# Kernel optimization log

Measured on AMD Instinct MI355X. Metric: run time of the kernel, lower is better.

Reference implementation:

```python
import jax, jax.numpy as jnp
import numpy as np

NUM_CLASSES = 1
STRIDES = (8, 16, 32)
CENTER_RADIUS = 2.5
REG_W, OBJ_W, CLS_W, LMK_W = 5.0, 1.0, 1.0, 5.0
BETA = 1.0 / 9.0   # SmoothL1 beta
BIG = 1e9          # mask-out cost for non-fg anchors / invalid GTs


def _bce_logits(x, t):
    # BCEWithLogits: softplus(x) - x*t (stable)
    return jax.nn.softplus(x) - x * t


def _smooth_l1(d):
    a = jnp.abs(d)
    return jnp.where(a < BETA, 0.5 * a * a / BETA, a - 0.5 * BETA)


def _make_grids(hw_list):
    gs, ss = [], []
    for (h, w), s in zip(hw_list, STRIDES):
        yv, xv = jnp.meshgrid(jnp.arange(h), jnp.arange(w), indexing='ij')
        g = jnp.stack([xv, yv], -1).reshape(-1, 2).astype(jnp.float32)
        gs.append(g)
        ss.append(jnp.full((g.shape[0],), float(s), jnp.float32))
    return jnp.concatenate(gs, 0), jnp.concatenate(ss, 0)


def _flat(p):
    b, c = p.shape[0], p.shape[1]
    return p.transpose(0, 2, 3, 1).reshape(b, -1, c)


def _pairwise_iou(a, b):
    # a [G,4] xyxy, b [A,4] xyxy -> [G,A]
    tl = jnp.maximum(a[:, None, :2], b[None, :, :2])
    br = jnp.minimum(a[:, None, 2:], b[None, :, 2:])
    wh = jnp.clip(br - tl, 0.0)
    inter = wh[..., 0] * wh[..., 1]
    aa = (a[:, 2] - a[:, 0]) * (a[:, 3] - a[:, 1])
    ab = (b[:, 2] - b[:, 0]) * (b[:, 3] - b[:, 1])
    return inter / (aa[:, None] + ab[None, :] - inter + 1e-8)


def _giou(a, b):
    # elementwise GIoU, a,b [N,4] xyxy -> [N]
    tl = jnp.maximum(a[:, :2], b[:, :2]); br = jnp.minimum(a[:, 2:], b[:, 2:])
    wh = jnp.clip(br - tl, 0.0); inter = wh[:, 0] * wh[:, 1]
    aa = (a[:, 2] - a[:, 0]) * (a[:, 3] - a[:, 1])
    ab = (b[:, 2] - b[:, 0]) * (b[:, 3] - b[:, 1])
    union = aa + ab - inter
    iou = inter / (union + 1e-8)
    ctl = jnp.minimum(a[:, :2], b[:, :2]); cbr = jnp.maximum(a[:, 2:], b[:, 2:])
    cwh = jnp.clip(cbr - ctl, 0.0); carea = cwh[:, 0] * cwh[:, 1]
    return iou - (carea - union) / (carea + 1e-8)


def _assign(boxes, cls, obj, gt_boxes, gt_labels, gt_valid, grids, strides):
    # SimOTA, masked/jittable form. boxes [A,4], cls [A,C], obj [A,1], gt_* [G,...]
    G = gt_boxes.shape[0]
    xys = (grids + 0.5) * strides[:, None]  # [A,2] anchor centers
    dl = xys[None, :, 0] - gt_boxes[:, None, 0]
    dr = gt_boxes[:, None, 2] - xys[None, :, 0]
    dt = xys[None, :, 1] - gt_boxes[:, None, 1]
    db = gt_boxes[:, None, 3] - xys[None, :, 1]
    in_box = (jnp.minimum(jnp.minimum(dl, dr), jnp.minimum(dt, db)) > 0.0) & gt_valid[:, None]
    cx = (gt_boxes[:, 0] + gt_boxes[:, 2]) * 0.5
    cy = (gt_boxes[:, 1] + gt_boxes[:, 3]) * 0.5
    rad = CENTER_RADIUS * strides[None, :]
    cdl = xys[None, :, 0] - (cx[:, None] - rad)
    cdr = cx[:, None] + rad - xys[None, :, 0]
    cdt = xys[None, :, 1] - (cy[:, None] - rad)
    cdb = cy[:, None] + rad - xys[None, :, 1]
    in_ctr = (jnp.minimum(jnp.minimum(cdl, cdr), jnp.minimum(cdt, cdb)) > 0.0) & gt_valid[:, None]
    fg = jnp.any(in_box, 0) | jnp.any(in_ctr, 0)  # [A] candidate anchors
    in_both = in_box & in_ctr
    ious = _pairwise_iou(gt_boxes, boxes) * fg[None, :].astype(boxes.dtype)  # [G,A]
    topk = jax.lax.top_k(ious, 10)[0]
    dyn_k = jnp.maximum(topk.sum(1).astype(jnp.int32), 1)  # dynamic-k per GT
    p = jnp.sqrt(jax.nn.sigmoid(cls) * jax.nn.sigmoid(obj))  # [A,C]
    t = jax.nn.one_hot(gt_labels, NUM_CLASSES)               # [G,C]
    logp = jnp.clip(jnp.log(p), -100.0)
    log1mp = jnp.clip(jnp.log(1.0 - p), -100.0)
    cls_cost = -(t[:, None, :] * logp[None] + (1.0 - t[:, None, :]) * log1mp[None]).sum(-1)
    cost = (cls_cost - 3.0 * jnp.log(ious + 1e-8)
            + 1e5 * (~in_both) + BIG * (~fg)[None, :] + BIG * (~gt_valid)[:, None])
    # rank-based smallest-k selection == topk(largest=False)
    ranks = jnp.argsort(jnp.argsort(cost, 1), 1)
    matching = (ranks < dyn_k[:, None]) & fg[None, :] & gt_valid[:, None]
    # conflict resolution: anchor matched to >1 GT keeps argmin-cost GT
    multi = matching.sum(0) > 1
    keep = jnp.arange(G)[:, None] == jnp.argmin(cost, 0)[None, :]
    matching = jnp.where(multi[None, :], keep, matching)
    fg_final = jnp.any(matching, 0)
    matched_gt = jnp.argmax(matching, 0)
    pred_ious = (matching.astype(boxes.dtype) * ious).sum(0)
    return fg_final, matched_gt, pred_ious


def _image_loss(boxes, cls, obj, lmk, gt_boxes, gt_labels, gt_lmk, gt_valid, grids, strides):
    fg, mgt, pious = _assign(boxes, cls, obj, gt_boxes, gt_labels, gt_valid, grids, strides)
    fgf = fg.astype(boxes.dtype)
    loss_obj = _bce_logits(obj[:, 0], fgf).sum()
    cls_t = jax.nn.one_hot(gt_labels[mgt], NUM_CLASSES) * pious[:, None]
    loss_cls = (_bce_logits(cls, cls_t) * fgf[:, None]).sum()
    loss_iou = ((1.0 - _giou(boxes, gt_boxes[mgt])) * fgf).sum()
    lmk_t = gt_lmk[mgt]  # [A,5,2]
    vm = ((lmk_t[..., 0] >= 0) & (lmk_t[..., 1] >= 0) & fg[:, None]).astype(boxes.dtype)
    loss_lmk = (_smooth_l1(lmk - lmk_t) * vm[..., None]).sum() / jnp.maximum(vm.sum(), 1.0)
    return loss_iou, loss_obj, loss_cls, loss_lmk, fgf.sum()


def _forward(cls0, reg0, obj0, lmk0, cls1, reg1, obj1, lmk1, cls2, reg2, obj2, lmk2,
             gt_boxes, gt_landmarks, gt_labels, gt_valid):
    hw = [(c.shape[2], c.shape[3]) for c in (cls0, cls1, cls2)]
    grids, strides = _make_grids(hw)
    cls_p = jnp.concatenate([_flat(cls0), _flat(cls1), _flat(cls2)], 1)  # [B,A,C]
    reg_p = jnp.concatenate([_flat(reg0), _flat(reg1), _flat(reg2)], 1)  # [B,A,4]
    obj_p = jnp.concatenate([_flat(obj0), _flat(obj1), _flat(obj2)], 1)  # [B,A,1]
    lmk_p = jnp.concatenate([_flat(lmk0), _flat(lmk1), _flat(lmk2)], 1)  # [B,A,10]
    b, A = reg_p.shape[0], reg_p.shape[1]
    xy = (reg_p[..., :2] + grids[None]) * strides[None, :, None]
    wh = jnp.exp(reg_p[..., 2:]) * strides[None, :, None]
    boxes = jnp.concatenate([xy - 0.5 * wh, xy + 0.5 * wh], -1)  # xyxy [B,A,4]
    lmk = (lmk_p.reshape(b, A, 5, 2) + grids[None, :, None, :]) * strides[None, :, None, None]
    li, lo, lc, ll, nfg = jax.vmap(_image_loss, in_axes=(0, 0, 0, 0, 0, 0, 0, 0, None, None))(
        boxes, cls_p, obj_p, lmk, gt_boxes, gt_labels, gt_landmarks, gt_valid, grids, strides)
    num_fg = jnp.maximum(nfg.sum(), 1.0)
    liou = REG_W * li.sum() / num_fg
    lobj = OBJ_W * lo.sum() / num_fg
    lcls = CLS_W * lc.sum() / num_fg
    llmk = LMK_W * ll.sum() / num_fg
    return liou + lobj + lcls + llmk, liou, lobj, lcls, llmk


def setup_inputs() -> dict:
    key = jax.random.key(0)
    ks = jax.random.split(key, 18)
    B, G = 16, 50
    d = {}
    for i, (h, w) in enumerate([(80, 80), (40, 40), (20, 20)]):
        d[f'cls{i}'] = jax.random.normal(ks[4 * i + 0], (B, NUM_CLASSES, h, w), jnp.float32)
        d[f'reg{i}'] = jax.random.normal(ks[4 * i + 1], (B, 4, h, w), jnp.float32)
        d[f'obj{i}'] = jax.random.normal(ks[4 * i + 2], (B, 1, h, w), jnp.float32)
        d[f'lmk{i}'] = jax.random.normal(ks[4 * i + 3], (B, 10, h, w), jnp.float32)
    cx = jax.random.uniform(ks[12], (B, G), minval=48.0, maxval=592.0)
    cy = jax.random.uniform(ks[13], (B, G), minval=48.0, maxval=592.0)
    wd = jax.random.uniform(ks[14], (B, G, 2), minval=12.0, maxval=96.0)
    d['gt_boxes'] = jnp.stack([cx - wd[..., 0] / 2, cy - wd[..., 1] / 2,
                               cx + wd[..., 0] / 2, cy + wd[..., 1] / 2], -1)
    u = jax.random.uniform(ks[15], (B, G, 5, 2))
    pts = d['gt_boxes'][..., None, :2] + u * wd[..., None, :]
    inv = jax.random.uniform(ks[16], (B, G, 5)) < 0.15  # some invisible landmarks
    d['gt_landmarks'] = jnp.where(inv[..., None], -1.0, pts)
    d['gt_labels'] = jnp.zeros((B, G), jnp.int32)  # single class (face)
    d['gt_valid'] = jnp.ones((B, G), bool)
    return d


def reference(cls0, reg0, obj0, lmk0, cls1, reg1, obj1, lmk1, cls2, reg2, obj2, lmk2,
              gt_boxes, gt_landmarks, gt_labels, gt_valid):
    return _forward(cls0, reg0, obj0, lmk0, cls1, reg1, obj1, lmk1, cls2, reg2, obj2, lmk2,
                    gt_boxes, gt_landmarks, gt_labels, gt_valid)
```

## Files before the change

### kernel.cpp

```cpp
#include <hip/hip_runtime.h>
#include <math.h>

#define NB 16
#define NA 8400
#define NG 50
#define TK 10
#define SELT 256
#define LP 11
#define NCHUNK 33
#define FGB 2
#define MCAP 512

#define CTR_FG(b)  ((b)*64)
#define CTR_M(b)   ((b)*64 + 16)
#define CTR_FD     (16*64)

__device__ __forceinline__ float sigmoidf_(float x){ return 1.f/(1.f+expf(-x)); }
__device__ __forceinline__ float softplusf_(float x){ return log1pf(expf(-fabsf(x))) + fmaxf(x, 0.f); }
__device__ __forceinline__ float bce_(float x, float t){ return softplusf_(x) - x*t; }
__device__ __forceinline__ float sl1_(float d){
    const float B = 1.f/9.f;
    float a = fabsf(d);
    return a < B ? 0.5f*a*a/B : a - 0.5f*B;
}

__device__ __forceinline__ void anchor_geom(int a, int& lvl, int& hw, int& gx, int& gy, float& st){
    if (a < 6400){ lvl=0; hw=a;      gx=hw%80; gy=hw/80; st=8.f; }
    else if (a < 8000){ lvl=1; hw=a-6400; gx=hw%40; gy=hw/40; st=16.f; }
    else { lvl=2; hw=a-8000; gx=hw%20; gy=hw/20; st=32.f; }
}

__device__ __forceinline__ float giou_(float4 a, float4 b){
    float tlx = fmaxf(a.x,b.x), tly = fmaxf(a.y,b.y);
    float brx = fminf(a.z,b.z), bry = fminf(a.w,b.w);
    float iw = fmaxf(brx-tlx,0.f), ih = fmaxf(bry-tly,0.f);
    float inter = iw*ih;
    float aa = (a.z-a.x)*(a.w-a.y);
    float ab = (b.z-b.x)*(b.w-b.y);
    float uni = aa + ab - inter;
    float iou = inter / (uni + 1e-8f);
    float ctlx = fminf(a.x,b.x), ctly = fminf(a.y,b.y);
    float cbrx = fmaxf(a.z,b.z), cbry = fmaxf(a.w,b.w);
    float cw = fmaxf(cbrx-ctlx,0.f), ch = fmaxf(cbry-ctly,0.f);
    float ca = cw*ch;
    return iou - (ca - uni) / (ca + 1e-8f);
}

__global__ void __launch_bounds__(256) k_decode(
    const float* __restrict__ cls0, const float* __restrict__ reg0, const float* __restrict__ obj0, const float* __restrict__ lmk0,
    const float* __restrict__ cls1, const float* __restrict__ reg1, const float* __restrict__ obj1, const float* __restrict__ lmk1,
    const float* __restrict__ cls2, const float* __restrict__ reg2, const float* __restrict__ obj2, const float* __restrict__ lmk2,
    const float* __restrict__ gtb, const unsigned char* __restrict__ gtv_raw, unsigned char* __restrict__ gtv,
    int* __restrict__ fgList, int* __restrict__ posOf, int* __restrict__ ctr,
    float4* __restrict__ boxC, float4* __restrict__ metaC,
    float* __restrict__ ccPC, float* __restrict__ ccNC,
    float* __restrict__ lmkC, float2* __restrict__ ocC,
    int4* __restrict__ mstate, double* __restrict__ pObj)
{
    __shared__ float4 sgb[NG];
    __shared__ unsigned char sval[NG];
    __shared__ int sIsByte;
    __shared__ int swc[4];
    __shared__ int sbase;
    __shared__ double sred[256];
    int b = blockIdx.y;
    int tid = threadIdx.x;
    int a = blockIdx.x * 256 + tid;
    bool act = (a < NA);

    int lvl, hw, gx, gy; float st = 0.f;
    float rx=0.f, ry=0.f, rw=0.f, rh=0.f, cl=0.f, ob=0.f, lmv[10];
    #pragma unroll
    for (int k = 0; k < 10; k++) lmv[k] = 0.f;
    if (act){
        anchor_geom(a, lvl, hw, gx, gy, st);
        const float* cp = lvl==0?cls0:(lvl==1?cls1:cls2);
        const float* rp = lvl==0?reg0:(lvl==1?reg1:reg2);
        const float* op = lvl==0?obj0:(lvl==1?obj1:obj2);
        const float* lp = lvl==0?lmk0:(lvl==1?lmk1:lmk2);
        int HW = lvl==0?6400:(lvl==1?1600:400);
        rx = rp[(b*4+0)*HW+hw]; ry = rp[(b*4+1)*HW+hw];
        rw = rp[(b*4+2)*HW+hw]; rh = rp[(b*4+3)*HW+hw];
        cl = cp[b*HW+hw]; ob = op[b*HW+hw];
        #pragma unroll
        for (int k = 0; k < 10; k++) lmv[k] = lp[(b*10+k)*HW+hw];
    }

    if (tid == 0) sIsByte = 0;
    if (tid < NG){
        const float* gp = &gtb[(size_t)(b*NG+tid)*4];
        sgb[tid] = make_float4(gp[0], gp[1], gp[2], gp[3]);
    }
    __syncthreads();
    {
        int any = 0;
        for (int i = tid; i < NB*NG; i += 256) if ((i & 3) && gtv_raw[i]) any = 1;
        if (any) sIsByte = 1;
    }
    __syncthreads();
    if (tid < NG){
        unsigned char vv = sIsByte ? (gtv_raw[b*NG+tid] != 0) : (gtv_raw[4*(b*NG+tid)] != 0);
        sval[tid] = vv;
        if (blockIdx.x == 0) gtv[b*NG+tid] = vv;
    }
    __syncthreads();

    double so = 0.0;
    bool f = false;
    float4 bx; float ax=0.f, ay=0.f, r=0.f, abv=0.f, ccPv=0.f, ccNv=0.f;
    float lmc[10];
    if (act){
        int idx = b*NA + a;
        float xc = (rx + (float)gx) * st, yc = (ry + (float)gy) * st;
        float wd = expf(rw) * st, ht = expf(rh) * st;
        bx = make_float4(xc - 0.5f*wd, yc - 0.5f*ht, xc + 0.5f*wd, yc + 0.5f*ht);
        abv = (bx.z - bx.x) * (bx.w - bx.y);
        so = (double)softplusf_(ob);
        float p = sqrtf(sigmoidf_(cl) * sigmoidf_(ob));
        ccPv = -fmaxf(logf(p), -100.f);
        ccNv = -fmaxf(logf(1.f - p), -100.f);
        #pragma unroll
        for (int k = 0; k < 5; k++){
            lmc[2*k]   = (lmv[2*k]   + (float)gx) * st;
            lmc[2*k+1] = (lmv[2*k+1] + (float)gy) * st;
        }
        mstate[idx] = make_int4(0, 0x7fffffff, 0, 0);
        ax = ((float)gx + 0.5f) * st; ay = ((float)gy + 0.5f) * st;
        r = 2.5f * st;
        for (int g = 0; g < NG; g++){
            if (!__ballot(!f)) break;
            if (!sval[g]) continue;
            float4 gv = sgb[g];
            bool inb = fminf(fminf(ax-gv.x, gv.z-ax), fminf(ay-gv.y, gv.w-ay)) > 0.f;
            float cx = (gv.x+gv.z)*0.5f, cy = (gv.y+gv.w)*0.5f;
            bool inc = fminf(fminf(ax-(cx-r), (cx+r)-ax), fminf(ay-(cy-r), (cy+r)-ay)) > 0.f;
            f = f || inb || inc;
        }
    }

    unsigned long long m = __ballot(f);
    int wave = tid >> 6, lane = tid & 63;
    if (lane == 0) swc[wave] = __popcll(m);
    __syncthreads();
    if (tid == 0){
        int tot = swc[0] + swc[1] + swc[2] + swc[3];
        sbase = tot ? atomicAdd(&ctr[CTR_FG(b)], tot) : 0;
    }
    __syncthreads();
    if (f){
        int wbase = sbase;
        for (int w = 0; w < 4; w++) if (w < wave) wbase += swc[w];
        int pos = wbase + __popcll(m & ((1ull << lane) - 1ull));
        fgList[b*NA + pos] = a;
        posOf[b*NA + a] = pos;
        boxC[b*NA + pos] = bx;
        metaC[b*NA + pos] = make_float4(ax, ay, r, abv);
        ccPC[b*NA + pos] = ccPv;
        ccNC[b*NA + pos] = ccNv;
        ocC[b*NA + pos] = make_float2(ob, cl);
        #pragma unroll
        for (int k = 0; k < 10; k++) lmkC[(size_t)(b*NA + pos)*10 + k] = lmc[k];
    }

    sred[tid] = so;
    for (int off = 128; off >= 1; off >>= 1){
        __syncthreads();
        if (tid < off) sred[tid] += sred[tid+off];
    }
    if (tid == 0) pObj[b*NCHUNK + blockIdx.x] = sred[0];
}

__global__ void __launch_bounds__(SELT) k_select(
    const int* __restrict__ fgList, const int* __restrict__ posOf, int* __restrict__ ctr,
    const float4* __restrict__ boxC, const float4* __restrict__ metaC,
    const float* __restrict__ ccPC, const float* __restrict__ ccNC,
    const float* __restrict__ gtb, const int* __restrict__ gtl, const unsigned char* __restrict__ gtv,
    int4* __restrict__ mstate, int* __restrict__ mList)
{
    int bg = blockIdx.x;
    int b = bg / NG, g = bg - b*NG;
    if (!gtv[b*NG+g]) return;
    int tid = threadIdx.x;

    __shared__ float sIou[SELT*LP];
    __shared__ unsigned long long sK[SELT*LP];
    __shared__ int sDk;

    const float* gp = &gtb[(size_t)(b*NG+g)*4];
    float4 gb = make_float4(gp[0], gp[1], gp[2], gp[3]);
    bool lab0 = (gtl[b*NG+g] == 0);
    int nf = ctr[CTR_FG(b)];

    float ag = (gb.z - gb.x) * (gb.w - gb.y);
    float cx = (gb.x + gb.z) * 0.5f, cy = (gb.y + gb.w) * 0.5f;

    const float4* bC = boxC  + (size_t)b*NA;
    const float4* mC = metaC + (size_t)b*NA;
    const float*  cS = (lab0 ? ccPC : ccNC) + (size_t)b*NA;
    const int*    fL = fgList + (size_t)b*NA;

    float mi[TK]; unsigned long long mk[TK];
    #pragma unroll
    for (int k = 0; k < TK; k++){ mi[k] = 0.f; mk[k] = 0xFFFFFFFFFFFFFFFFull; }

    int i = tid;
    float4 bxv, mt; float ccv; unsigned int ia;
    if (i < nf){ bxv = bC[i]; mt = mC[i]; ccv = cS[i]; ia = (unsigned int)fL[i]; }
    while (i < nf){
        int i2 = i + SELT;
        float4 bxv2, mt2; float ccv2; unsigned int ia2;
        if (i2 < nf){ bxv2 = bC[i2]; mt2 = mC[i2]; ccv2 = cS[i2]; ia2 = (unsigned int)fL[i2]; }
        float tlx = fmaxf(gb.x, bxv.x), tly = fmaxf(gb.y, bxv.y);
        float brx = fminf(gb.z, bxv.z), bry = fminf(gb.w, bxv.w);
        float iw = fmaxf(brx - tlx, 0.f), ih = fmaxf(bry - tly, 0.f);
        float inter = iw * ih;
        float im = inter / (ag + mt.w - inter + 1e-8f);
        float ax = mt.x, ay = mt.y, r = mt.z;
        bool inb = fminf(fminf(ax-gb.x, gb.z-ax), fminf(ay-gb.y, gb.w-ay)) > 0.f;
        bool inc = fminf(fminf(ax-(cx-r), (cx+r)-ax), fminf(ay-(cy-r), (cy+r)-ay)) > 0.f;
        float c = ccv - 3.f * logf(im + 1e-8f);
        if (!(inb && inc)) c += 1e5f;
        if (im > mi[TK-1]){
            float v = im;
            #pragma unroll
            for (int k = 0; k < TK; k++){
                if (v > mi[k]){ float t = mi[k]; mi[k] = v; v = t; }
            }
        }
        unsigned int fb = __float_as_uint(c);
        unsigned int ck = fb ^ ((unsigned int)((int)fb >> 31) | 0x80000000u);
        unsigned long long key = ((unsigned long long)ck << 32) | ia;
        if (key < mk[TK-1]){
            unsigned long long kv = key;
            #pragma unroll
            for (int k = 0; k < TK; k++){
                if (kv < mk[k]){ unsigned long long t = mk[k]; mk[k] = kv; kv = t; }
            }
        }
        i = i2; bxv = bxv2; mt = mt2; ccv = ccv2; ia = ia2;
    }

    #pragma unroll
    for (int k = 0; k < TK; k++){
        sIou[tid*LP+k] = mi[k];
        sK[tid*LP+k] = mk[k];
    }

    for (int off = SELT/2; off >= 1; off >>= 1){
        __syncthreads();
        if (tid < off){
            {
                float* Al = &sIou[tid*LP]; float* Bl = &sIou[(tid+off)*LP];
                float r2[TK]; int ii = 0, jj = 0;
                for (int k = 0; k < TK; k++){
                    bool ta = (jj >= TK) || (ii < TK && Al[ii] >= Bl[jj]);
                    r2[k] = ta ? Al[ii++] : Bl[jj++];
                }
                for (int k = 0; k < TK; k++) Al[k] = r2[k];
            }
            {
                unsigned long long* Ak = &sK[tid*LP]; unsigned long long* Bk = &sK[(tid+off)*LP];
                unsigned long long rk[TK]; int ii = 0, jj = 0;
                for (int k = 0; k < TK; k++){
                    bool ta = (jj >= TK) || (ii < TK && Ak[ii] <= Bk[jj]);
                    rk[k] = ta ? Ak[ii++] : Bk[jj++];
                }
                for (int k = 0; k < TK; k++) Ak[k] = rk[k];
            }
        }
    }
    __syncthreads();
    if (tid == 0){
        float s = 0.f;
        for (int k = 0; k < TK; k++) s += sIou[k];
        int dk = (int)s;
        if (dk < 1) dk = 1;
        if (dk > TK) dk = TK;
        sDk = dk;
    }
    __syncthreads();
    int dk = sDk;
    if (tid < dk){
        unsigned long long kk = sK[tid];
        unsigned int a = (unsigned int)(kk & 0xFFFFFFFFull);
        if (a < (unsigned int)NA){
            int pos = posOf[b*NA + (int)a];
            int* mp = (int*)&mstate[b*NA + (int)a];
            int old = atomicAdd(mp, 1);
            if (old == 0){
                int p = atomicAdd(&ctr[CTR_M(b)], 1);
                mList[b*MCAP + p] = (int)a;
            }
            atomicMin(mp + 1, g);
            float4 bxv = boxC[b*NA + pos];
            float4 mt = metaC[b*NA + pos];
            float tlx = fmaxf(gb.x, bxv.x), tly = fmaxf(gb.y, bxv.y);
            float brx = fminf(gb.z, bxv.z), bry = fminf(gb.w, bxv.w);
            float iw = fmaxf(brx - tlx, 0.f), ih = fmaxf(bry - tly, 0.f);
            float inter = iw * ih;
            float im = inter / (ag + mt.w - inter + 1e-8f);
            atomicAdd((float*)(mp + 2), im);
        }
    }
}

__global__ void __launch_bounds__(256) k_fg_loss(
    const float4* __restrict__ boxC, const float4* __restrict__ metaC,
    const float* __restrict__ ccPC, const float* __restrict__ ccNC,
    const float* __restrict__ lmkC, const float2* __restrict__ ocC,
    const int* __restrict__ posOf, const int4* __restrict__ mstate,
    const int* __restrict__ mList, int* __restrict__ ctr,
    const float* __restrict__ gtb, const float* __restrict__ gtlm, const int* __restrict__ gtl,
    const unsigned char* __restrict__ gtv, double* __restrict__ partials,
    const double* __restrict__ pObj, float* __restrict__ out)
{
    __shared__ float4 sgb[NG];
    __shared__ int slab[NG];
    __shared__ unsigned char sval[NG];
    __shared__ float slmk[NG*10];
    int b = blockIdx.y;
    int tid = threadIdx.x;
    if (tid < NG){
        const float* gp = &gtb[(size_t)(b*NG+tid)*4];
        sgb[tid] = make_float4(gp[0], gp[1], gp[2], gp[3]);
        slab[tid] = gtl[b*NG+tid];
        sval[tid] = gtv[b*NG+tid];
    }
    for (int i = tid; i < NG*10; i += 256) slmk[i] = gtlm[(size_t)b*NG*10 + i];
    __syncthreads();

    int n = ctr[CTR_M(b)];
    double lo = 0, lc = 0, li = 0, lnum = 0, lden = 0, nfg = 0;

    for (int i = blockIdx.x*256 + tid; i < n; i += FGB*256){
        int a = mList[b*MCAP + i];
        int pos = posOf[b*NA + a];
        int4 ms = mstate[b*NA + a];
        float4 bx = boxC[b*NA + pos];
        float4 mt = metaC[b*NA + pos];
        float2 oc = ocC[b*NA + pos];
        float pious; int m;
        if (ms.x == 1){ m = ms.y; pious = __int_as_float(ms.z); }
        else {
            float ax = mt.x, ay = mt.y, r = mt.z, ab = mt.w;
            float cp = ccPC[b*NA + pos], cn = ccNC[b*NA + pos];
            float bestC = INFINITY, bestIou = 0.f; int bestG = 0;
            for (int g = 0; g < NG; g++){
                float4 gbv = sgb[g];
                int valid = sval[g];
                float tlx = fmaxf(gbv.x, bx.x), tly = fmaxf(gbv.y, bx.y);
                float brx = fminf(gbv.z, bx.z), bry = fminf(gbv.w, bx.w);
                float iw = fmaxf(brx - tlx, 0.f), ih = fmaxf(bry - tly, 0.f);
                float inter = iw * ih;
                float agv = (gbv.z - gbv.x) * (gbv.w - gbv.y);
                float im = inter / (agv + ab - inter + 1e-8f);
                bool inb = (fminf(fminf(ax-gbv.x, gbv.z-ax), fminf(ay-gbv.y, gbv.w-ay)) > 0.f) && valid;
                float cxg = (gbv.x + gbv.z) * 0.5f, cyg = (gbv.y + gbv.w) * 0.5f;
                bool inc = (fminf(fminf(ax-(cxg-r), (cxg+r)-ax), fminf(ay-(cyg-r), (cyg+r)-ay)) > 0.f) && valid;
                float cc = (slab[g] == 0) ? cp : cn;
                float c = cc - 3.f * logf(im + 1e-8f);
                if (!(inb && inc)) c += 1e5f;
                if (!valid) c += 1e9f;
                if (c < bestC){ bestC = c; bestG = g; bestIou = im; }
            }
            m = bestG; pious = bestIou;
        }
        lo += (double)(-oc.x);
        float tgt = (slab[m] == 0) ? pious : 0.f;
        lc += (double)bce_(oc.y, tgt);
        li += (double)(1.f - giou_(bx, sgb[m]));
        #pragma unroll
        for (int k = 0; k < 5; k++){
            float tx = slmk[m*10 + 2*k];
            float ty = slmk[m*10 + 2*k + 1];
            if (tx >= 0.f && ty >= 0.f){
                lnum += (double)(sl1_(lmkC[(size_t)(b*NA+pos)*10 + 2*k] - tx)
                               + sl1_(lmkC[(size_t)(b*NA+pos)*10 + 2*k + 1] - ty));
                lden += 1.0;
            }
        }
        nfg += 1.0;
    }

    __shared__ double s[6*256];
    s[0*256+tid] = lo; s[1*256+tid] = lc; s[2*256+tid] = li;
    s[3*256+tid] = lnum; s[4*256+tid] = lden; s[5*256+tid] = nfg;
    for (int off = 128; off >= 1; off >>= 1){
        __syncthreads();
        if (tid < off){
            #pragma unroll
            for (int q = 0; q < 6; q++) s[q*256+tid] += s[q*256+tid+off];
        }
    }
    if (tid == 0){
        #pragma unroll
        for (int q = 0; q < 6; q++) partials[(b*FGB + blockIdx.x)*6 + q] = s[q*256];
    }

    __threadfence();
    __shared__ int sLast;
    if (tid == 0) sLast = (atomicAdd(&ctr[CTR_FD], 1) == NB*FGB - 1);
    __syncthreads();
    if (!sLast) return;

    __shared__ double sf[NB][5];
    if (tid < NB){
        double flo = 0, flc = 0, fli = 0, fln = 0, fld = 0, fnf = 0;
        for (int ch = 0; ch < NCHUNK; ch++) flo += pObj[tid*NCHUNK + ch];
        for (int blk = 0; blk < FGB; blk++){
            const double* p = &partials[(tid*FGB + blk)*6];
            flo += p[0]; flc += p[1]; fli += p[2];
            fln += p[3]; fld += p[4]; fnf += p[5];
        }
        sf[tid][0] = flo; sf[tid][1] = flc; sf[tid][2] = fli;
        sf[tid][3] = fln / fmax(fld, 1.0); sf[tid][4] = fnf;
    }
    __syncthreads();
    if (tid == 0){
        double flo = 0, flc = 0, fli = 0, fll = 0, fnfg = 0;
        for (int bb = 0; bb < NB; bb++){
            flo += sf[bb][0]; flc += sf[bb][1]; fli += sf[bb][2]; fll += sf[bb][3]; fnfg += sf[bb][4];
        }
        double nf2 = fmax(fnfg, 1.0);
        double liou = 5.0 * fli / nf2;
        double lobj = 1.0 * flo / nf2;
        double lcls = 1.0 * flc / nf2;
        double llmk = 5.0 * fll / nf2;
        out[0] = (float)(liou + lobj + lcls + llmk);
        out[1] = (float)liou;
        out[2] = (float)lobj;
        out[3] = (float)lcls;
        out[4] = (float)llmk;
    }
}

extern "C" void kernel_launch(void* const* d_in, const int* in_sizes, int n_in,
                              void* d_out, int out_size, void* d_ws, size_t ws_size,
                              hipStream_t stream) {
    const float* cls0 = (const float*)d_in[0];
    const float* reg0 = (const float*)d_in[1];
    const float* obj0 = (const float*)d_in[2];
    const float* lmk0 = (const float*)d_in[3];
    const float* cls1 = (const float*)d_in[4];
    const float* reg1 = (const float*)d_in[5];
    const float* obj1 = (const float*)d_in[6];
    const float* lmk1 = (const float*)d_in[7];
    const float* cls2 = (const float*)d_in[8];
    const float* reg2 = (const float*)d_in[9];
    const float* obj2 = (const float*)d_in[10];
    const float* lmk2 = (const float*)d_in[11];
    const float* gtb  = (const float*)d_in[12];
    const float* gtlm = (const float*)d_in[13];
    const int*   gtl  = (const int*)d_in[14];
    const unsigned char* gtv_raw = (const unsigned char*)d_in[15];
    float* out = (float*)d_out;

    char* ws = (char*)d_ws;
    size_t off = 0;
    float4* boxC  = (float4*)(ws + off); off += (size_t)NB*NA*sizeof(float4);
    float4* metaC = (float4*)(ws + off); off += (size_t)NB*NA*sizeof(float4);
    int4* mstate  = (int4*)(ws + off);   off += (size_t)NB*NA*sizeof(int4);
    float* lmkC = (float*)(ws + off); off += (size_t)NB*NA*10*sizeof(float);
    float2* ocC = (float2*)(ws + off); off += (size_t)NB*NA*sizeof(float2);
    float* ccPC = (float*)(ws + off); off += (size_t)NB*NA*sizeof(float);
    float* ccNC = (float*)(ws + off); off += (size_t)NB*NA*sizeof(float);
    int* fgList = (int*)(ws + off);   off += (size_t)NB*NA*sizeof(int);
    int* posOf  = (int*)(ws + off);   off += (size_t)NB*NA*sizeof(int);
    int* mList  = (int*)(ws + off);   off += (size_t)NB*MCAP*sizeof(int);
    int* ctr    = (int*)(ws + off);   off += (size_t)8192;
    double* pObj = (double*)(ws + off); off += (size_t)NB*NCHUNK*sizeof(double);
    double* partials = (double*)(ws + off); off += (size_t)NB*FGB*6*sizeof(double);
    unsigned char* gtv = (unsigned char*)(ws + off); off += (size_t)NB*NG;

    hipMemsetAsync(ctr, 0, 8192, stream);

    dim3 grdA(NCHUNK, NB);
    k_decode<<<grdA, dim3(256), 0, stream>>>(cls0, reg0, obj0, lmk0, cls1, reg1, obj1, lmk1,
                                             cls2, reg2, obj2, lmk2, gtb, gtv_raw, gtv,
                                             fgList, posOf, ctr, boxC, metaC, ccPC, ccNC,
                                             lmkC, ocC, mstate, pObj);

    k_select<<<dim3(NB*NG), dim3(SELT), 0, stream>>>(fgList, posOf, ctr, boxC, metaC, ccPC, ccNC,
                                                     gtb, gtl, gtv, mstate, mList);

    k_fg_loss<<<dim3(FGB, NB), dim3(256), 0, stream>>>(boxC, metaC, ccPC, ccNC, lmkC, ocC,
                                                       posOf, mstate, mList, ctr,
                                                       gtb, gtlm, gtl, gtv, partials,
                                                       pObj, out);
}
```

Before: 76.75 us.

## Compact mstate by fg position, transpose landmark buffer, deepen select prefetch

Result: slower. 79.21 us (+3.2%).

```diff
diff --git a/kernel.cpp b/kernel.cpp
--- a/kernel.cpp
+++ b/kernel.cpp
@@ -110,7 +110,6 @@
     float4 bx; float ax=0.f, ay=0.f, r=0.f, abv=0.f, ccPv=0.f, ccNv=0.f;
     float lmc[10];
     if (act){
-        int idx = b*NA + a;
         float xc = (rx + (float)gx) * st, yc = (ry + (float)gy) * st;
         float wd = expf(rw) * st, ht = expf(rh) * st;
         bx = make_float4(xc - 0.5f*wd, yc - 0.5f*ht, xc + 0.5f*wd, yc + 0.5f*ht);
@@ -124,7 +123,6 @@
             lmc[2*k]   = (lmv[2*k]   + (float)gx) * st;
             lmc[2*k+1] = (lmv[2*k+1] + (float)gy) * st;
         }
-        mstate[idx] = make_int4(0, 0x7fffffff, 0, 0);
         ax = ((float)gx + 0.5f) * st; ay = ((float)gy + 0.5f) * st;
         r = 2.5f * st;
         for (int g = 0; g < NG; g++){
@@ -158,8 +156,9 @@
         ccPC[b*NA + pos] = ccPv;
         ccNC[b*NA + pos] = ccNv;
         ocC[b*NA + pos] = make_float2(ob, cl);
+        mstate[b*NA + pos] = make_int4(0, 0x7fffffff, 0, 0);
         #pragma unroll
-        for (int k = 0; k < 10; k++) lmkC[(size_t)(b*NA + pos)*10 + k] = lmc[k];
+        for (int k = 0; k < 10; k++) lmkC[(size_t)k*(NB*NA) + b*NA + pos] = lmc[k];
     }
 
     sred[tid] = so;
@@ -203,13 +202,7 @@
     #pragma unroll
     for (int k = 0; k < TK; k++){ mi[k] = 0.f; mk[k] = 0xFFFFFFFFFFFFFFFFull; }
 
-    int i = tid;
-    float4 bxv, mt; float ccv; unsigned int ia;
-    if (i < nf){ bxv = bC[i]; mt = mC[i]; ccv = cS[i]; ia = (unsigned int)fL[i]; }
-    while (i < nf){
-        int i2 = i + SELT;
-        float4 bxv2, mt2; float ccv2; unsigned int ia2;
-        if (i2 < nf){ bxv2 = bC[i2]; mt2 = mC[i2]; ccv2 = cS[i2]; ia2 = (unsigned int)fL[i2]; }
+    auto PROC = [&](float4 bxv, float4 mt, float ccv, unsigned int ia){
         float tlx = fmaxf(gb.x, bxv.x), tly = fmaxf(gb.y, bxv.y);
         float brx = fminf(gb.z, bxv.z), bry = fminf(gb.w, bxv.w);
         float iw = fmaxf(brx - tlx, 0.f), ih = fmaxf(bry - tly, 0.f);
@@ -237,7 +230,22 @@
                 if (kv < mk[k]){ unsigned long long t = mk[k]; mk[k] = kv; kv = t; }
             }
         }
-        i = i2; bxv = bxv2; mt = mt2; ccv = ccv2; ia = ia2;
+    };
+
+    int i = tid;
+    float4 bxA, mtA, bxB, mtB; float ccA = 0.f, ccB = 0.f; unsigned int iaA = 0, iaB = 0;
+    if (i < nf)        { bxA = bC[i];        mtA = mC[i];        ccA = cS[i];        iaA = (unsigned int)fL[i]; }
+    if (i + SELT < nf) { bxB = bC[i+SELT];   mtB = mC[i+SELT];   ccB = cS[i+SELT];   iaB = (unsigned int)fL[i+SELT]; }
+    while (i < nf){
+        int iC = i + 2*SELT, iD = i + 3*SELT;
+        float4 bxCn, mtCn, bxDn, mtDn; float ccCn = 0.f, ccDn = 0.f; unsigned int iaCn = 0, iaDn = 0;
+        if (iC < nf){ bxCn = bC[iC]; mtCn = mC[iC]; ccCn = cS[iC]; iaCn = (unsigned int)fL[iC]; }
+        if (iD < nf){ bxDn = bC[iD]; mtDn = mC[iD]; ccDn = cS[iD]; iaDn = (unsigned int)fL[iD]; }
+        PROC(bxA, mtA, ccA, iaA);
+        if (i + SELT < nf) PROC(bxB, mtB, ccB, iaB);
+        i = iC;
+        bxA = bxCn; mtA = mtCn; ccA = ccCn; iaA = iaCn;
+        bxB = bxDn; mtB = mtDn; ccB = ccDn; iaB = iaDn;
     }
 
     #pragma unroll
@@ -285,7 +293,7 @@
         unsigned int a = (unsigned int)(kk & 0xFFFFFFFFull);
         if (a < (unsigned int)NA){
             int pos = posOf[b*NA + (int)a];
-            int* mp = (int*)&mstate[b*NA + (int)a];
+            int* mp = (int*)&mstate[b*NA + pos];
             int old = atomicAdd(mp, 1);
             if (old == 0){
                 int p = atomicAdd(&ctr[CTR_M(b)], 1);
@@ -335,7 +343,7 @@
     for (int i = blockIdx.x*256 + tid; i < n; i += FGB*256){
         int a = mList[b*MCAP + i];
         int pos = posOf[b*NA + a];
-        int4 ms = mstate[b*NA + a];
+        int4 ms = mstate[b*NA + pos];
         float4 bx = boxC[b*NA + pos];
         float4 mt = metaC[b*NA + pos];
         float2 oc = ocC[b*NA + pos];
@@ -374,8 +382,8 @@
             float tx = slmk[m*10 + 2*k];
             float ty = slmk[m*10 + 2*k + 1];
             if (tx >= 0.f && ty >= 0.f){
-                lnum += (double)(sl1_(lmkC[(size_t)(b*NA+pos)*10 + 2*k] - tx)
-                               + sl1_(lmkC[(size_t)(b*NA+pos)*10 + 2*k + 1] - ty));
+                lnum += (double)(sl1_(lmkC[(size_t)(2*k)*(NB*NA) + b*NA + pos] - tx)
+                               + sl1_(lmkC[(size_t)(2*k+1)*(NB*NA) + b*NA + pos] - ty));
                 lden += 1.0;
             }
         }
```
